# Kernel optimization log

Hardware: AMD Instinct MI355X
Metric: run time of the kernel (lower is better)

The kernel has to match this reference:

```python
import jax, jax.numpy as jnp
import numpy as np

N, E, H, D_IN, D_OUT, DEPTH, G = 100000, 1600000, 128, 128, 10, 3, 256


def setup_inputs() -> dict:
    key = jax.random.key(0)
    ks = jax.random.split(key, 16)
    s = lambda k, shape: jax.random.normal(k, shape, dtype=jnp.float32) * 0.05
    inp = {
        "x": jax.random.normal(ks[0], (N, D_IN), dtype=jnp.float32),
        "edge_index": jax.random.randint(ks[1], (2, E), 0, N, dtype=jnp.int32),
        "control_edge_index": jax.random.randint(ks[2], (2, 1024), 0, N, dtype=jnp.int32),
        "batch": jnp.sort(jax.random.randint(ks[3], (N,), 0, G, dtype=jnp.int32)),
        # encoder MLP: input_dim -> hidden -> hidden
        "enc_w1": s(ks[4], (D_IN, H)), "enc_b1": jnp.zeros((H,), jnp.float32),
        "enc_w2": s(ks[5], (H, H)),    "enc_b2": jnp.zeros((H,), jnp.float32),
        # conv_depth GCN layers, hidden -> hidden
        "conv_w": s(ks[6], (DEPTH, H, H)), "conv_b": jnp.zeros((DEPTH, H), jnp.float32),
        # decoder MLP: hidden -> hidden -> output_dim
        "dec_w1": s(ks[7], (H, H)),     "dec_b1": jnp.zeros((H,), jnp.float32),
        "dec_w2": s(ks[8], (H, D_OUT)), "dec_b2": jnp.zeros((D_OUT,), jnp.float32),
    }
    return inp


def _gcn_forward(x, enc_w1, enc_b1, enc_w2, enc_b2, conv_w, conv_b,
                 dec_w1, dec_b1, dec_w2, dec_b2, edge_index, batch):
    # encoder MLP (Linear-ReLU-Dropout(eval)-Linear)
    h = jax.nn.relu(x @ enc_w1 + enc_b1) @ enc_w2 + enc_b2

    # GCN normalization with self-loops: D^{-1/2} (A + I) D^{-1/2}
    loops = jnp.arange(N, dtype=edge_index.dtype)
    src = jnp.concatenate([edge_index[0], loops])  # [E + N]
    dst = jnp.concatenate([edge_index[1], loops])
    deg = jax.ops.segment_sum(jnp.ones_like(src, dtype=h.dtype), dst, num_segments=N)
    inv_sqrt = jax.lax.rsqrt(deg)  # deg >= 1 thanks to self-loops
    coef = (inv_sqrt[src] * inv_sqrt[dst])[:, None]  # [E+N, 1]

    for l in range(DEPTH):
        hw = h @ conv_w[l] + conv_b[l]                      # [N, H]
        h = jax.ops.segment_sum(hw[src] * coef, dst, num_segments=N)
        if l < DEPTH - 1:  # linear=False -> nonlinearity between convs
            h = jax.nn.relu(h)

    # global_add_pool over graph ids
    pooled = jax.ops.segment_sum(h, batch, num_segments=G)   # [G, H]

    # decoder MLP
    return jax.nn.relu(pooled @ dec_w1 + dec_b1) @ dec_w2 + dec_b2  # [G, D_OUT]


def reference(x, edge_index, control_edge_index, batch, enc_w1, enc_b1, enc_w2,
              enc_b2, conv_w, conv_b, dec_w1, dec_b1, dec_w2, dec_b2):
    # control_edge_index corresponds to the (disabled) control mechanism; unused
    return _gcn_forward(x, enc_w1, enc_b1, enc_w2, enc_b2, conv_w, conv_b,
                        dec_w1, dec_b1, dec_w2, dec_b2, edge_index, batch)
```

## Files before the change

### kernel.cpp

```cpp
#include <hip/hip_runtime.h>
#include <hip/hip_bf16.h>
#include <cstdint>
#include <cstddef>

#define NN 100000
#define NE 1600000
#define HH 128
#define NG 256

#define NB 196
#define BSH 9
#define BMSK 511
#define CHUNK 4096
#define NBLK 391
#define GB 782
#define NBK 391

typedef __bf16 bf16x8 __attribute__((ext_vector_type(8)));
typedef float floatx4 __attribute__((ext_vector_type(4)));

__device__ __forceinline__ uint32_t f2b(float f) {
  union { float f; uint32_t u; } v; v.f = f;
  uint32_t u = v.u;
  return (u + 0x7FFFu + ((u >> 16) & 1u)) >> 16;
}
__device__ __forceinline__ float blo(uint32_t u) {
  union { uint32_t u; float f; } v; v.u = u << 16;
  return v.f;
}
__device__ __forceinline__ float bhi(uint32_t u) {
  union { uint32_t u; float f; } v; v.u = u & 0xFFFF0000u;
  return v.f;
}
__device__ __forceinline__ void addrow(float* a, uint4 v) {
  a[0] += blo(v.x); a[1] += bhi(v.x);
  a[2] += blo(v.y); a[3] += bhi(v.y);
  a[4] += blo(v.z); a[5] += bhi(v.z);
  a[6] += blo(v.w); a[7] += bhi(v.w);
}

__device__ __forceinline__ void stage_w(uint16_t (*Wt)[136], const float* __restrict__ W,
                                        int tid) {
  for (int it = 0; it < 16; ++it) {
    int idx = tid + it * 256;
    int n = idx & 127;
    int k0 = (idx >> 7) * 4;
    uint2 wv;
    wv.x = f2b(W[(k0 + 0) * 128 + n]) | (f2b(W[(k0 + 1) * 128 + n]) << 16);
    wv.y = f2b(W[(k0 + 2) * 128 + n]) | (f2b(W[(k0 + 3) * 128 + n]) << 16);
    *(uint2*)&Wt[n][k0] = wv;
  }
}

__global__ __launch_bounds__(256) void k_front(const int* __restrict__ src,
                                               int* __restrict__ blkcnt,
                                               const float* __restrict__ conv_w,
                                               uint16_t* __restrict__ wbf) {
  int t = threadIdx.x;
  if (blockIdx.x < NBLK) {
    __shared__ int h[NB];
    if (t < NB) h[t] = 0;
    __syncthreads();
    int base = blockIdx.x * CHUNK, end = min(base + CHUNK, NE);
    for (int i = base + t; i < end; i += 256) atomicAdd(&h[src[i] >> BSH], 1);
    __syncthreads();
    if (t < NB) blkcnt[blockIdx.x * NB + t] = h[t];
  } else {
    int idx = (blockIdx.x - NBLK) * 256 + t;
    int l = idx >> 14;
    int n = (idx >> 7) & 127;
    int k = idx & 127;
    wbf[idx] = (uint16_t)f2b(conv_w[(l + 1) * 16384 + k * 128 + n]);
  }
}

__global__ __launch_bounds__(256) void k_cntB(const uint2* __restrict__ pairs,
                                              int* __restrict__ blkcnt) {
  __shared__ int h[NB];
  int t = threadIdx.x;
  if (t < NB) h[t] = 0;
  __syncthreads();
  int base = blockIdx.x * CHUNK, end = min(base + CHUNK, NE);
  for (int i = base + t; i < end; i += 256) atomicAdd(&h[pairs[i].y >> BSH], 1);
  __syncthreads();
  if (t < NB) blkcnt[blockIdx.x * NB + t] = h[t];
}

__global__ void k_scan(const int* __restrict__ blkcnt, int* __restrict__ poff,
                       int* __restrict__ gbase, int* __restrict__ off, int set_off) {
  __shared__ int s[256];
  int t = threadIdx.x;
  int tot = 0;
  if (t < NB) {
    for (int r = 0; r < NBLK; ++r) {
      poff[r * NB + t] = tot;
      tot += blkcnt[r * NB + t];
    }
  }
  s[t] = (t < NB) ? tot : 0;
  __syncthreads();
  for (int d = 1; d < 256; d <<= 1) {
    int v = (t >= d) ? s[t - d] : 0;
    __syncthreads();
    s[t] += v;
    __syncthreads();
  }
  if (t < NB) gbase[t] = s[t] - tot;
  if (t == 0) { gbase[NB] = NE; if (set_off) off[NN] = NE; }
}

__global__ __launch_bounds__(256) void k_placeA(const int* __restrict__ src,
                                                const int* __restrict__ dst,
                                                const int* __restrict__ poff,
                                                const int* __restrict__ gbase,
                                                uint2* __restrict__ pairs) {
  __shared__ int cur[NB];
  int t = threadIdx.x;
  if (t < NB) cur[t] = poff[blockIdx.x * NB + t] + gbase[t];
  __syncthreads();
  int base = blockIdx.x * CHUNK, end = min(base + CHUNK, NE);
  for (int i = base + t; i < end; i += 256) {
    int s = src[i], d = dst[i];
    int p = atomicAdd(&cur[s >> BSH], 1);
    pairs[p] = make_uint2((unsigned)s, (unsigned)d);
  }
}

__global__ __launch_bounds__(256) void k_placeB(const uint2* __restrict__ pairs,
                                                const int* __restrict__ poff,
                                                const int* __restrict__ gbase,
                                                uint32_t* __restrict__ outb) {
  __shared__ int cur[NB];
  int t = threadIdx.x;
  if (t < NB) cur[t] = poff[blockIdx.x * NB + t] + gbase[t];
  __syncthreads();
  int base = blockIdx.x * CHUNK, end = min(base + CHUNK, NE);
  for (int i = base + t; i < end; i += 256) {
    uint2 v = pairs[i];
    int p = atomicAdd(&cur[v.y >> BSH], 1);
    outb[p] = v.x | ((v.y & (unsigned)BMSK) << 17);
  }
}

__global__ __launch_bounds__(256) void k_sortenc(
    const uint32_t* __restrict__ pairbuf, const int* __restrict__ gbase,
    const int* __restrict__ batch,
    int* __restrict__ off, int* __restrict__ csrs,
    int* __restrict__ dhist2, int* __restrict__ gstart,
    const float* __restrict__ A32, const float* __restrict__ W,
    const float* __restrict__ bias, uint16_t* __restrict__ Out)
{
  __shared__ char smraw[34816];
  const int tid = threadIdx.x;

  if (blockIdx.x < GB) {
    auto Wt = (uint16_t(*)[136])smraw;
    stage_w(Wt, W, tid);
    __syncthreads();

    const int lane = tid & 63;
    const int wave = tid >> 6;
    const int lrow = lane & 15;
    const int quad = lane >> 4;
    const int lk = quad * 8;
    const int row0 = blockIdx.x * 128 + wave * 32;

    floatx4 acc[2][8];
#pragma unroll
    for (int t = 0; t < 2; ++t)
#pragma unroll
      for (int n = 0; n < 8; ++n)
        acc[t][n] = (floatx4){0.f, 0.f, 0.f, 0.f};

#pragma unroll
    for (int ks = 0; ks < 4; ++ks) {
      bf16x8 a[2];
#pragma unroll
      for (int t = 0; t < 2; ++t) {
        int r = row0 + t * 16 + lrow;
        uint4 tmp = {0u, 0u, 0u, 0u};
        if (r < NN) {
          float4 f0 = *(const float4*)(A32 + (size_t)r * HH + ks * 32 + lk);
          float4 f1 = *(const float4*)(A32 + (size_t)r * HH + ks * 32 + lk + 4);
          tmp.x = f2b(f0.x) | (f2b(f0.y) << 16);
          tmp.y = f2b(f0.z) | (f2b(f0.w) << 16);
          tmp.z = f2b(f1.x) | (f2b(f1.y) << 16);
          tmp.w = f2b(f1.z) | (f2b(f1.w) << 16);
        }
        a[t] = __builtin_bit_cast(bf16x8, tmp);
      }
#pragma unroll
      for (int n = 0; n < 8; ++n) {
        bf16x8 b = __builtin_bit_cast(bf16x8, *(const uint4*)&Wt[n * 16 + lrow][ks * 32 + lk]);
        acc[0][n] = __builtin_amdgcn_mfma_f32_16x16x32_bf16(b, a[0], acc[0][n], 0, 0, 0);
        acc[1][n] = __builtin_amdgcn_mfma_f32_16x16x32_bf16(b, a[1], acc[1][n], 0, 0, 0);
      }
    }

    float4 b4[8];
#pragma unroll
    for (int n = 0; n < 8; ++n) b4[n] = *(const float4*)(bias + n * 16 + quad * 4);

#pragma unroll
    for (int t = 0; t < 2; ++t) {
      int row = row0 + t * 16 + lrow;
      if (row < NN) {
        uint16_t* orow = Out + (size_t)row * HH;
#pragma unroll
        for (int n = 0; n < 8; ++n) {
          float v0 = fmaxf(acc[t][n][0] + b4[n].x, 0.f);
          float v1 = fmaxf(acc[t][n][1] + b4[n].y, 0.f);
          float v2 = fmaxf(acc[t][n][2] + b4[n].z, 0.f);
          float v3 = fmaxf(acc[t][n][3] + b4[n].w, 0.f);
          uint2 o;
          o.x = f2b(v0) | (f2b(v1) << 16);
          o.y = f2b(v2) | (f2b(v3) << 16);
          *(uint2*)(orow + n * 16 + quad * 4) = o;
        }
      }
    }
  } else {
    int* cnt  = (int*)smraw;
    int* loff = cnt + 512;
    int* psum = loff + 512;
    int b = blockIdx.x - GB;
    cnt[tid] = 0; cnt[tid + 256] = 0;
    __syncthreads();
    int s0 = gbase[b], s1 = gbase[b + 1];
    for (int i = s0 + tid; i < s1; i += 256)
      atomicAdd(&cnt[pairbuf[i] >> 17], 1);
    __syncthreads();
    int a0 = cnt[2 * tid], a1 = cnt[2 * tid + 1];
    int s = a0 + a1;
    psum[tid] = s;
    __syncthreads();
    for (int d = 1; d < 256; d <<= 1) {
      int v = (tid >= d) ? psum[tid - d] : 0;
      __syncthreads();
      psum[tid] += v;
      __syncthreads();
    }
    int excl = psum[tid] - s;
    loff[2 * tid] = excl;
    loff[2 * tid + 1] = excl + a0;
    __syncthreads();
    int* h64 = psum;
    if (tid < 64) h64[tid] = 0;
    __syncthreads();
#pragma unroll
    for (int k = 0; k < 2; ++k) {
      int i = tid + k * 256;
      int node = b * 512 + i;
      if (node < NN) {
        off[node] = s0 + loff[i];
        int d = cnt[i]; if (d > 63) d = 63;
        atomicAdd(&h64[d], 1);
      }
    }
    {
      int n0 = b * 512, n1 = min(n0 + 512, NN);
      for (int i = n0 + tid; i < n1; i += 256) {
        int bb = batch[i];
        if (i == 0) { for (int g = 0; g <= bb; ++g) gstart[g] = 0; }
        else { int aa = batch[i - 1]; for (int g = aa + 1; g <= bb; ++g) gstart[g] = i; }
        if (i == NN - 1) { for (int g = bb + 1; g <= NG; ++g) gstart[g] = NN; }
      }
    }
    __syncthreads();
    if (tid < 64) dhist2[b * 64 + tid] = h64[tid];
    cnt[tid] = loff[tid]; cnt[tid + 256] = loff[tid + 256];
    __syncthreads();
    for (int i = s0 + tid; i < s1; i += 256) {
      uint32_t v = pairbuf[i];
      int p = atomicAdd(&cnt[v >> 17], 1);
      csrs[s0 + p] = (int)(v & 0x1FFFFu);
    }
  }
}

__global__ __launch_bounds__(256) void k_dinv(const int* __restrict__ dhist2,
                                              int* __restrict__ dcur,
                                              const int* __restrict__ off,
                                              float* __restrict__ inv) {
  if (blockIdx.x == 0) {
    int t = threadIdx.x;
    if (t < 64) {
      int sum = 0;
      for (int r = 0; r < NB; ++r) sum += dhist2[r * 64 + (63 - t)];
      int v = sum;
      for (int d = 1; d < 64; d <<= 1) { int u = __shfl_up(v, d); if (t >= d) v += u; }
      dcur[63 - t] = v - sum;
    }
  } else {
    int i = (blockIdx.x - 1) * 256 + threadIdx.x;
    if (i < NN) inv[i] = rsqrtf((float)(off[i + 1] - off[i]) + 1.0f);
  }
}

__global__ __launch_bounds__(256) void k_dualplace(
    const uint16_t* __restrict__ A16,
    const float* __restrict__ Wa, const float* __restrict__ ba,
    const float* __restrict__ Wb, const float* __restrict__ bb,
    const float* __restrict__ scale, uint16_t* __restrict__ Out,
    const int* __restrict__ off, int* __restrict__ dcur, int* __restrict__ order)
{
  __shared__ uint16_t Wt[128][136];
  __shared__ uint16_t tile[128][136];
  const int tid = threadIdx.x;

  if (blockIdx.x < GB) {
    stage_w(Wt, Wa, tid);
    __syncthreads();

    const int lane = tid & 63;
    const int wave = tid >> 6;
    const int lrow = lane & 15;
    const int quad = lane >> 4;
    const int lk = quad * 8;
    const int row0 = blockIdx.x * 128 + wave * 32;
    const int trow0 = wave * 32;

    floatx4 acc[2][8];
#pragma unroll
    for (int t = 0; t < 2; ++t)
#pragma unroll
      for (int n = 0; n < 8; ++n)
        acc[t][n] = (floatx4){0.f, 0.f, 0.f, 0.f};

#pragma unroll
    for (int ks = 0; ks < 4; ++ks) {
      bf16x8 a[2];
#pragma unroll
      for (int t = 0; t < 2; ++t) {
        int r = row0 + t * 16 + lrow;
        uint4 tmp = {0u, 0u, 0u, 0u};
        if (r < NN) tmp = *(const uint4*)(A16 + (size_t)r * HH + ks * 32 + lk);
        a[t] = __builtin_bit_cast(bf16x8, tmp);
      }
#pragma unroll
      for (int n = 0; n < 8; ++n) {
        bf16x8 b = __builtin_bit_cast(bf16x8, *(const uint4*)&Wt[n * 16 + lrow][ks * 32 + lk]);
        acc[0][n] = __builtin_amdgcn_mfma_f32_16x16x32_bf16(b, a[0], acc[0][n], 0, 0, 0);
        acc[1][n] = __builtin_amdgcn_mfma_f32_16x16x32_bf16(b, a[1], acc[1][n], 0, 0, 0);
      }
    }

    {
      float4 b4[8];
#pragma unroll
      for (int n = 0; n < 8; ++n) b4[n] = *(const float4*)(ba + n * 16 + quad * 4);
#pragma unroll
      for (int t = 0; t < 2; ++t) {
        int trow = trow0 + t * 16 + lrow;
#pragma unroll
        for (int n = 0; n < 8; ++n) {
          uint2 o;
          o.x = f2b(acc[t][n][0] + b4[n].x) | (f2b(acc[t][n][1] + b4[n].y) << 16);
          o.y = f2b(acc[t][n][2] + b4[n].z) | (f2b(acc[t][n][3] + b4[n].w) << 16);
          *(uint2*)&tile[trow][n * 16 + quad * 4] = o;
        }
      }
    }
    __syncthreads();
    stage_w(Wt, Wb, tid);
#pragma unroll
    for (int t = 0; t < 2; ++t)
#pragma unroll
      for (int n = 0; n < 8; ++n)
        acc[t][n] = (floatx4){0.f, 0.f, 0.f, 0.f};
    __syncthreads();

#pragma unroll
    for (int ks = 0; ks < 4; ++ks) {
      bf16x8 a[2];
#pragma unroll
      for (int t = 0; t < 2; ++t)
        a[t] = __builtin_bit_cast(bf16x8,
                 *(const uint4*)&tile[trow0 + t * 16 + lrow][ks * 32 + lk]);
#pragma unroll
      for (int n = 0; n < 8; ++n) {
        bf16x8 b = __builtin_bit_cast(bf16x8, *(const uint4*)&Wt[n * 16 + lrow][ks * 32 + lk]);
        acc[0][n] = __builtin_amdgcn_mfma_f32_16x16x32_bf16(b, a[0], acc[0][n], 0, 0, 0);
        acc[1][n] = __builtin_amdgcn_mfma_f32_16x16x32_bf16(b, a[1], acc[1][n], 0, 0, 0);
      }
    }

    {
      float4 b4[8];
#pragma unroll
      for (int n = 0; n < 8; ++n) b4[n] = *(const float4*)(bb + n * 16 + quad * 4);
#pragma unroll
      for (int t = 0; t < 2; ++t) {
        int row = row0 + t * 16 + lrow;
        if (row < NN) {
          float sc = scale[row];
          uint16_t* orow = Out + (size_t)row * HH;
#pragma unroll
          for (int n = 0; n < 8; ++n) {
            float v0 = (acc[t][n][0] + b4[n].x) * sc;
            float v1 = (acc[t][n][1] + b4[n].y) * sc;
            float v2 = (acc[t][n][2] + b4[n].z) * sc;
            float v3 = (acc[t][n][3] + b4[n].w) * sc;
            uint2 o;
            o.x = f2b(v0) | (f2b(v1) << 16);
            o.y = f2b(v2) | (f2b(v3) << 16);
            *(uint2*)(orow + n * 16 + quad * 4) = o;
          }
        }
      }
    }
  } else {
    int* h = (int*)Wt;
    int* base = h + 64;
    if (tid < 64) h[tid] = 0;
    __syncthreads();
    int i = (blockIdx.x - GB) * 256 + tid;
    int d = 0, ld = 0;
    if (i < NN) { d = off[i + 1] - off[i]; if (d > 63) d = 63; ld = atomicAdd(&h[d], 1); }
    __syncthreads();
    if (tid < 64) base[tid] = h[tid] ? atomicAdd(&dcur[tid], h[tid]) : 0;
    __syncthreads();
    if (i < NN) order[base[d] + ld] = i;
  }
}

__global__ __launch_bounds__(256) void k_agg(
    const uint16_t* __restrict__ hw2, const int* __restrict__ off,
    const int* __restrict__ csrs, const float* __restrict__ inv,
    const int* __restrict__ order,
    uint16_t* __restrict__ hout, int do_relu)
{
  int slot = blockIdx.x * 16 + (threadIdx.x >> 4);
  if (slot >= NN) return;
  int node = order[slot];
  int c = (threadIdx.x & 15) * 8;
  const uint16_t* rowp = hw2 + c;

  uint4 sv = *(const uint4*)(rowp + (size_t)node * HH);
  float a[8] = {0.f, 0.f, 0.f, 0.f, 0.f, 0.f, 0.f, 0.f};
  addrow(a, sv);

  int e0 = off[node], e1 = off[node + 1];
  int e = e0;
  for (; e + 4 <= e1; e += 4) {
    int s0 = csrs[e + 0], s1 = csrs[e + 1], s2 = csrs[e + 2], s3 = csrs[e + 3];
    uint4 v0 = *(const uint4*)(rowp + (size_t)s0 * HH);
    uint4 v1 = *(const uint4*)(rowp + (size_t)s1 * HH);
    uint4 v2 = *(const uint4*)(rowp + (size_t)s2 * HH);
    uint4 v3 = *(const uint4*)(rowp + (size_t)s3 * HH);
    addrow(a, v0); addrow(a, v1); addrow(a, v2); addrow(a, v3);
  }
  for (; e < e1; ++e) {
    int s = csrs[e];
    uint4 v = *(const uint4*)(rowp + (size_t)s * HH);
    addrow(a, v);
  }
  float invd = inv[node];
#pragma unroll
  for (int j = 0; j < 8; ++j) {
    a[j] *= invd;
    if (do_relu) a[j] = fmaxf(a[j], 0.f);
  }
  uint4 o;
  o.x = f2b(a[0]) | (f2b(a[1]) << 16);
  o.y = f2b(a[2]) | (f2b(a[3]) << 16);
  o.z = f2b(a[4]) | (f2b(a[5]) << 16);
  o.w = f2b(a[6]) | (f2b(a[7]) << 16);
  *(uint4*)(hout + (size_t)node * HH + c) = o;
}

__global__ __launch_bounds__(512) void k_aggemm(
    const uint16_t* __restrict__ hw2, const int* __restrict__ off,
    const int* __restrict__ csrs, const float* __restrict__ inv,
    const int* __restrict__ order,
    const uint16_t* __restrict__ Wbf, const float* __restrict__ bias,
    uint16_t* __restrict__ Out)
{
  __shared__ uint4 S4[32][16];
  __shared__ int nid[32];
  const int tid = threadIdx.x;

  const int group = tid >> 4;
  const int node = order[blockIdx.x * 32 + group];
  const int c = (tid & 15) * 8;
  if ((tid & 15) == 0) nid[group] = node;
  const uint16_t* rowp = hw2 + c;

  uint4 sv = *(const uint4*)(rowp + (size_t)node * HH);
  float a[8] = {0.f, 0.f, 0.f, 0.f, 0.f, 0.f, 0.f, 0.f};
  addrow(a, sv);

  int e0 = off[node], e1 = off[node + 1];
  int e = e0;
  for (; e + 4 <= e1; e += 4) {
    int s0 = csrs[e + 0], s1 = csrs[e + 1], s2 = csrs[e + 2], s3 = csrs[e + 3];
    uint4 v0 = *(const uint4*)(rowp + (size_t)s0 * HH);
    uint4 v1 = *(const uint4*)(rowp + (size_t)s1 * HH);
    uint4 v2 = *(const uint4*)(rowp + (size_t)s2 * HH);
    uint4 v3 = *(const uint4*)(rowp + (size_t)s3 * HH);
    addrow(a, v0); addrow(a, v1); addrow(a, v2); addrow(a, v3);
  }
  for (; e < e1; ++e) {
    int s = csrs[e];
    uint4 v = *(const uint4*)(rowp + (size_t)s * HH);
    addrow(a, v);
  }
  float invd = inv[node];
#pragma unroll
  for (int j = 0; j < 8; ++j) a[j] = fmaxf(a[j] * invd, 0.f);
  {
    uint4 o;
    o.x = f2b(a[0]) | (f2b(a[1]) << 16);
    o.y = f2b(a[2]) | (f2b(a[3]) << 16);
    o.z = f2b(a[4]) | (f2b(a[5]) << 16);
    o.w = f2b(a[6]) | (f2b(a[7]) << 16);
    S4[group][(tid & 15) ^ (group & 15)] = o;
  }
  __syncthreads();

  const int lane = tid & 63;
  const int wave = tid >> 6;
  const int lrow = lane & 15;
  const int quad = lane >> 4;
  const int lk = quad * 8;
  const uint16_t* wrow = Wbf + (size_t)(wave * 16 + lrow) * HH;

  floatx4 acc0 = (floatx4){0.f, 0.f, 0.f, 0.f};
  floatx4 acc1 = (floatx4){0.f, 0.f, 0.f, 0.f};
#pragma unroll
  for (int ks = 0; ks < 4; ++ks) {
    int ch = (ks * 4 + quad) ^ lrow;
    bf16x8 a0 = __builtin_bit_cast(bf16x8, S4[lrow][ch]);
    bf16x8 a1 = __builtin_bit_cast(bf16x8, S4[16 + lrow][ch]);
    bf16x8 b  = __builtin_bit_cast(bf16x8, *(const uint4*)(wrow + ks * 32 + lk));
    acc0 = __builtin_amdgcn_mfma_f32_16x16x32_bf16(b, a0, acc0, 0, 0, 0);
    acc1 = __builtin_amdgcn_mfma_f32_16x16x32_bf16(b, a1, acc1, 0, 0, 0);
  }

  float4 b4 = *(const float4*)(bias + wave * 16 + quad * 4);
#pragma unroll
  for (int t = 0; t < 2; ++t) {
    floatx4 ac = t ? acc1 : acc0;
    int row = nid[t * 16 + lrow];
    float sc = inv[row];
    float v0 = (ac[0] + b4.x) * sc;
    float v1 = (ac[1] + b4.y) * sc;
    float v2 = (ac[2] + b4.z) * sc;
    float v3 = (ac[3] + b4.w) * sc;
    uint2 o;
    o.x = f2b(v0) | (f2b(v1) << 16);
    o.y = f2b(v2) | (f2b(v3) << 16);
    *(uint2*)(Out + (size_t)row * HH + wave * 16 + quad * 4) = o;
  }
}

__global__ __launch_bounds__(256) void k_pooldec(
    const uint16_t* __restrict__ h, const int* __restrict__ gstart,
    const float* __restrict__ w1, const float* __restrict__ b1,
    const float* __restrict__ w2, const float* __restrict__ b2,
    float* __restrict__ out)
{
  __shared__ float red[16][132];
  __shared__ float p[128], tmpv[128];
  int g = blockIdx.x;
  int tid = threadIdx.x;
  int slot = tid >> 4;
  int c = (tid & 15) * 8;

  int r0 = gstart[g], r1 = gstart[g + 1];
  float a[8] = {0.f, 0.f, 0.f, 0.f, 0.f, 0.f, 0.f, 0.f};
  for (int r = r0 + slot; r < r1; r += 16) {
    uint4 v = *(const uint4*)(h + (size_t)r * HH + c);
    addrow(a, v);
  }
  *(float4*)&red[slot][c]     = make_float4(a[0], a[1], a[2], a[3]);
  *(float4*)&red[slot][c + 4] = make_float4(a[4], a[5], a[6], a[7]);
  __syncthreads();
  if (tid < 128) {
    float s = 0.f;
#pragma unroll
    for (int k = 0; k < 16; ++k) s += red[k][tid];
    p[tid] = s;
  }
  __syncthreads();
  if (tid < 128) {
    float acc1 = b1[tid];
    for (int k = 0; k < 128; ++k) acc1 += p[k] * w1[k * 128 + tid];
    tmpv[tid] = fmaxf(acc1, 0.f);
  }
  __syncthreads();
  if (tid < 10) {
    float o = b2[tid];
    for (int k = 0; k < 128; ++k) o += tmpv[k] * w2[k * 10 + tid];
    out[g * 10 + tid] = o;
  }
}

extern "C" void kernel_launch(void* const* d_in, const int* in_sizes, int n_in,
                              void* d_out, int out_size, void* d_ws, size_t ws_size,
                              hipStream_t stream) {
  const float* x       = (const float*)d_in[0];
  const int*   eidx    = (const int*)d_in[1];
  const int*   src     = eidx;
  const int*   dst     = eidx + NE;
  const int*   batch   = (const int*)d_in[3];
  const float* enc_w1  = (const float*)d_in[4];
  const float* enc_b1  = (const float*)d_in[5];
  const float* enc_w2  = (const float*)d_in[6];
  const float* enc_b2  = (const float*)d_in[7];
  const float* conv_w  = (const float*)d_in[8];
  const float* conv_b  = (const float*)d_in[9];
  const float* dec_w1  = (const float*)d_in[10];
  const float* dec_b1  = (const float*)d_in[11];
  const float* dec_w2  = (const float*)d_in[12];
  const float* dec_b2  = (const float*)d_in[13];
  float* out = (float*)d_out;

  char* ws = (char*)d_ws;
  size_t o = 0;
  auto alloc = [&](size_t bytes) -> char* {
    char* p = ws + o;
    o += (bytes + 255) & ~(size_t)255;
    return p;
  };
  int*      off     = (int*)alloc((size_t)(NN + 1) * 4);
  int*      csrs    = (int*)alloc((size_t)NE * 4);
  float*    inv     = (float*)alloc((size_t)NN * 4);
  int*      blkcntA = (int*)alloc((size_t)NBLK * NB * 4);
  int*      poffA   = (int*)alloc((size_t)NBLK * NB * 4);
  int*      blkcntB = (int*)alloc((size_t)NBLK * NB * 4);
  int*      poffB   = (int*)alloc((size_t)NBLK * NB * 4);
  int*      gbaseA  = (int*)alloc((size_t)(NB + 1) * 4);
  int*      gbaseB  = (int*)alloc((size_t)(NB + 1) * 4);
  int*      dhist2  = (int*)alloc((size_t)NB * 64 * 4);
  int*      dcur    = (int*)alloc(64 * 4);
  int*      order   = (int*)alloc((size_t)NN * 4);
  int*      gstart  = (int*)alloc((size_t)(NG + 1) * 4);
  uint16_t* wbf     = (uint16_t*)alloc((size_t)2 * 16384 * 2);
  uint32_t* pairB   = (uint32_t*)alloc((size_t)NE * 4);
  uint16_t* buf0    = (uint16_t*)alloc((size_t)NN * HH * 2);
  uint16_t* buf1    = (uint16_t*)alloc((size_t)NN * HH * 2);
  uint2*    pairsA  = (uint2*)buf1;

  k_front<<<dim3(NBLK + 128), dim3(256), 0, stream>>>(src, blkcntA, conv_w, wbf);
  k_scan<<<dim3(1), dim3(256), 0, stream>>>(blkcntA, poffA, gbaseA, off, 0);
  k_placeA<<<dim3(NBLK), dim3(256), 0, stream>>>(src, dst, poffA, gbaseA, pairsA);
  k_cntB<<<dim3(NBLK), dim3(256), 0, stream>>>(pairsA, blkcntB);
  k_scan<<<dim3(1), dim3(256), 0, stream>>>(blkcntB, poffB, gbaseB, off, 1);
  k_placeB<<<dim3(NBLK), dim3(256), 0, stream>>>(pairsA, poffB, gbaseB, pairB);
  k_sortenc<<<dim3(GB + NB), dim3(256), 0, stream>>>(pairB, gbaseB, batch, off, csrs,
                                                     dhist2, gstart,
                                                     x, enc_w1, enc_b1, buf1);
  k_dinv<<<dim3(1 + NBK), dim3(256), 0, stream>>>(dhist2, dcur, off, inv);
  k_dualplace<<<dim3(GB + NBK), dim3(256), 0, stream>>>(buf1, enc_w2, enc_b2,
                                                        conv_w + 0 * 16384, conv_b + 0,
                                                        inv, buf0, off, dcur, order);

  const int FB = NN / 32;
  const int AB = (NN + 15) / 16;
  k_aggemm<<<dim3(FB), dim3(512), 0, stream>>>(buf0, off, csrs, inv, order,
                                               wbf, conv_b + 128, buf1);
  k_aggemm<<<dim3(FB), dim3(512), 0, stream>>>(buf1, off, csrs, inv, order,
                                               wbf + 16384, conv_b + 256, buf0);
  k_agg <<<dim3(AB), dim3(256), 0, stream>>>(buf0, off, csrs, inv, order, buf1, 0);

  k_pooldec<<<dim3(NG), dim3(256), 0, stream>>>(buf1, gstart, dec_w1, dec_b1, dec_w2, dec_b2, out);
}
```

Baseline: 484.5 us.

## Fuse final aggregation with global add pooling via atomics; preload MFMA weights

The last GCN aggregation now accumulates directly into a float pooled buffer. Each block of 16 consecutive nodes forms per-graph partial sums in shared memory and adds them with atomics, so the bf16 write and re-read of the final node features is gone. The pooled buffer is zeroed inside the front kernel, and the decoder kernel now only reads the pooled rows. Separately, k_aggemm loads its weight fragments into registers before the gather phase so their latency overlaps the gather. The trade-offs are float atomics with nondeterministic summation order, and the loss of degree-sorted node ordering in the last aggregation.

```diff
diff --git a/kernel.cpp b/kernel.cpp
--- a/kernel.cpp
+++ b/kernel.cpp
@@ -55,7 +55,8 @@
 __global__ __launch_bounds__(256) void k_front(const int* __restrict__ src,
                                                int* __restrict__ blkcnt,
                                                const float* __restrict__ conv_w,
-                                               uint16_t* __restrict__ wbf) {
+                                               uint16_t* __restrict__ wbf,
+                                               float* __restrict__ pooled) {
   int t = threadIdx.x;
   if (blockIdx.x < NBLK) {
     __shared__ int h[NB];
@@ -65,12 +66,15 @@
     for (int i = base + t; i < end; i += 256) atomicAdd(&h[src[i] >> BSH], 1);
     __syncthreads();
     if (t < NB) blkcnt[blockIdx.x * NB + t] = h[t];
-  } else {
+  } else if (blockIdx.x < NBLK + 128) {
     int idx = (blockIdx.x - NBLK) * 256 + t;
     int l = idx >> 14;
     int n = (idx >> 7) & 127;
     int k = idx & 127;
     wbf[idx] = (uint16_t)f2b(conv_w[(l + 1) * 16384 + k * 128 + n]);
+  } else {
+    int i = ((blockIdx.x - NBLK - 128) * 256 + t) * 4;
+    if (i < NG * HH) *(float4*)&pooled[i] = make_float4(0.f, 0.f, 0.f, 0.f);
   }
 }
 
@@ -424,51 +428,6 @@
   }
 }
 
-__global__ __launch_bounds__(256) void k_agg(
-    const uint16_t* __restrict__ hw2, const int* __restrict__ off,
-    const int* __restrict__ csrs, const float* __restrict__ inv,
-    const int* __restrict__ order,
-    uint16_t* __restrict__ hout, int do_relu)
-{
-  int slot = blockIdx.x * 16 + (threadIdx.x >> 4);
-  if (slot >= NN) return;
-  int node = order[slot];
-  int c = (threadIdx.x & 15) * 8;
-  const uint16_t* rowp = hw2 + c;
-
-  uint4 sv = *(const uint4*)(rowp + (size_t)node * HH);
-  float a[8] = {0.f, 0.f, 0.f, 0.f, 0.f, 0.f, 0.f, 0.f};
-  addrow(a, sv);
-
-  int e0 = off[node], e1 = off[node + 1];
-  int e = e0;
-  for (; e + 4 <= e1; e += 4) {
-    int s0 = csrs[e + 0], s1 = csrs[e + 1], s2 = csrs[e + 2], s3 = csrs[e + 3];
-    uint4 v0 = *(const uint4*)(rowp + (size_t)s0 * HH);
-    uint4 v1 = *(const uint4*)(rowp + (size_t)s1 * HH);
-    uint4 v2 = *(const uint4*)(rowp + (size_t)s2 * HH);
-    uint4 v3 = *(const uint4*)(rowp + (size_t)s3 * HH);
-    addrow(a, v0); addrow(a, v1); addrow(a, v2); addrow(a, v3);
-  }
-  for (; e < e1; ++e) {
-    int s = csrs[e];
-    uint4 v = *(const uint4*)(rowp + (size_t)s * HH);
-    addrow(a, v);
-  }
-  float invd = inv[node];
-#pragma unroll
-  for (int j = 0; j < 8; ++j) {
-    a[j] *= invd;
-    if (do_relu) a[j] = fmaxf(a[j], 0.f);
-  }
-  uint4 o;
-  o.x = f2b(a[0]) | (f2b(a[1]) << 16);
-  o.y = f2b(a[2]) | (f2b(a[3]) << 16);
-  o.z = f2b(a[4]) | (f2b(a[5]) << 16);
-  o.w = f2b(a[6]) | (f2b(a[7]) << 16);
-  *(uint4*)(hout + (size_t)node * HH + c) = o;
-}
-
 __global__ __launch_bounds__(512) void k_aggemm(
     const uint16_t* __restrict__ hw2, const int* __restrict__ off,
     const int* __restrict__ csrs, const float* __restrict__ inv,
@@ -479,6 +438,17 @@
   __shared__ uint4 S4[32][16];
   __shared__ int nid[32];
   const int tid = threadIdx.x;
+  const int lane = tid & 63;
+  const int wave = tid >> 6;
+  const int lrow = lane & 15;
+  const int quad = lane >> 4;
+  const int lk = quad * 8;
+
+  const uint16_t* wrow = Wbf + (size_t)(wave * 16 + lrow) * HH;
+  uint4 w0 = *(const uint4*)(wrow + 0 * 32 + lk);
+  uint4 w1 = *(const uint4*)(wrow + 1 * 32 + lk);
+  uint4 w2 = *(const uint4*)(wrow + 2 * 32 + lk);
+  uint4 w3 = *(const uint4*)(wrow + 3 * 32 + lk);
 
   const int group = tid >> 4;
   const int node = order[blockIdx.x * 32 + group];
@@ -518,13 +488,6 @@
   }
   __syncthreads();
 
-  const int lane = tid & 63;
-  const int wave = tid >> 6;
-  const int lrow = lane & 15;
-  const int quad = lane >> 4;
-  const int lk = quad * 8;
-  const uint16_t* wrow = Wbf + (size_t)(wave * 16 + lrow) * HH;
-
   floatx4 acc0 = (floatx4){0.f, 0.f, 0.f, 0.f};
   floatx4 acc1 = (floatx4){0.f, 0.f, 0.f, 0.f};
 #pragma unroll
@@ -532,7 +495,8 @@
     int ch = (ks * 4 + quad) ^ lrow;
     bf16x8 a0 = __builtin_bit_cast(bf16x8, S4[lrow][ch]);
     bf16x8 a1 = __builtin_bit_cast(bf16x8, S4[16 + lrow][ch]);
-    bf16x8 b  = __builtin_bit_cast(bf16x8, *(const uint4*)(wrow + ks * 32 + lk));
+    uint4 wv = (ks == 0) ? w0 : (ks == 1) ? w1 : (ks == 2) ? w2 : w3;
+    bf16x8 b  = __builtin_bit_cast(bf16x8, wv);
     acc0 = __builtin_amdgcn_mfma_f32_16x16x32_bf16(b, a0, acc0, 0, 0, 0);
     acc1 = __builtin_amdgcn_mfma_f32_16x16x32_bf16(b, a1, acc1, 0, 0, 0);
   }
@@ -554,34 +518,72 @@
   }
 }
 
-__global__ __launch_bounds__(256) void k_pooldec(
-    const uint16_t* __restrict__ h, const int* __restrict__ gstart,
+__global__ __launch_bounds__(256) void k_aggpool(
+    const uint16_t* __restrict__ hw2, const int* __restrict__ off,
+    const int* __restrict__ csrs, const float* __restrict__ inv,
+    const int* __restrict__ batch,
+    float* __restrict__ pooled)
+{
+  __shared__ float red[16][132];
+  __shared__ int gid[16];
+  const int tid = threadIdx.x;
+  const int slot = tid >> 4;
+  const int node = blockIdx.x * 16 + slot;
+  const int c = (tid & 15) * 8;
+  if ((tid & 15) == 0) gid[slot] = batch[node];
+  const uint16_t* rowp = hw2 + c;
+
+  uint4 sv = *(const uint4*)(rowp + (size_t)node * HH);
+  float a[8] = {0.f, 0.f, 0.f, 0.f, 0.f, 0.f, 0.f, 0.f};
+  addrow(a, sv);
+
+  int e0 = off[node], e1 = off[node + 1];
+  int e = e0;
+  for (; e + 4 <= e1; e += 4) {
+    int s0 = csrs[e + 0], s1 = csrs[e + 1], s2 = csrs[e + 2], s3 = csrs[e + 3];
+    uint4 v0 = *(const uint4*)(rowp + (size_t)s0 * HH);
+    uint4 v1 = *(const uint4*)(rowp + (size_t)s1 * HH);
+    uint4 v2 = *(const uint4*)(rowp + (size_t)s2 * HH);
+    uint4 v3 = *(const uint4*)(rowp + (size_t)s3 * HH);
+    addrow(a, v0); addrow(a, v1); addrow(a, v2); addrow(a, v3);
+  }
+  for (; e < e1; ++e) {
+    int s = csrs[e];
+    uint4 v = *(const uint4*)(rowp + (size_t)s * HH);
+    addrow(a, v);
+  }
+  float invd = inv[node];
+#pragma unroll
+  for (int j = 0; j < 8; ++j) a[j] *= invd;
+  *(float4*)&red[slot][c]     = make_float4(a[0], a[1], a[2], a[3]);
+  *(float4*)&red[slot][c + 4] = make_float4(a[4], a[5], a[6], a[7]);
+  __syncthreads();
+
+  if (tid < 128) {
+    int g = gid[0];
+    float run = red[0][tid];
+    for (int r = 1; r < 16; ++r) {
+      int gg = gid[r];
+      if (gg != g) {
+        unsafeAtomicAdd(&pooled[(size_t)g * HH + tid], run);
+        run = 0.f; g = gg;
+      }
+      run += red[r][tid];
+    }
+    unsafeAtomicAdd(&pooled[(size_t)g * HH + tid], run);
+  }
+}
+
+__global__ __launch_bounds__(256) void k_dec(
+    const float* __restrict__ pooled,
     const float* __restrict__ w1, const float* __restrict__ b1,
     const float* __restrict__ w2, const float* __restrict__ b2,
     float* __restrict__ out)
 {
-  __shared__ float red[16][132];
   __shared__ float p[128], tmpv[128];
   int g = blockIdx.x;
   int tid = threadIdx.x;
-  int slot = tid >> 4;
-  int c = (tid & 15) * 8;
-
-  int r0 = gstart[g], r1 = gstart[g + 1];
-  float a[8] = {0.f, 0.f, 0.f, 0.f, 0.f, 0.f, 0.f, 0.f};
-  for (int r = r0 + slot; r < r1; r += 16) {
-    uint4 v = *(const uint4*)(h + (size_t)r * HH + c);
-    addrow(a, v);
-  }
-  *(float4*)&red[slot][c]     = make_float4(a[0], a[1], a[2], a[3]);
-  *(float4*)&red[slot][c + 4] = make_float4(a[4], a[5], a[6], a[7]);
-  __syncthreads();
-  if (tid < 128) {
-    float s = 0.f;
-#pragma unroll
-    for (int k = 0; k < 16; ++k) s += red[k][tid];
-    p[tid] = s;
-  }
+  if (tid < 128) p[tid] = pooled[(size_t)g * HH + tid];
   __syncthreads();
   if (tid < 128) {
     float acc1 = b1[tid];
@@ -636,13 +638,14 @@
   int*      dcur    = (int*)alloc(64 * 4);
   int*      order   = (int*)alloc((size_t)NN * 4);
   int*      gstart  = (int*)alloc((size_t)(NG + 1) * 4);
+  float*    pooled  = (float*)alloc((size_t)NG * HH * 4);
   uint16_t* wbf     = (uint16_t*)alloc((size_t)2 * 16384 * 2);
   uint32_t* pairB   = (uint32_t*)alloc((size_t)NE * 4);
   uint16_t* buf0    = (uint16_t*)alloc((size_t)NN * HH * 2);
   uint16_t* buf1    = (uint16_t*)alloc((size_t)NN * HH * 2);
   uint2*    pairsA  = (uint2*)buf1;
 
-  k_front<<<dim3(NBLK + 128), dim3(256), 0, stream>>>(src, blkcntA, conv_w, wbf);
+  k_front<<<dim3(NBLK + 128 + 32), dim3(256), 0, stream>>>(src, blkcntA, conv_w, wbf, pooled);
   k_scan<<<dim3(1), dim3(256), 0, stream>>>(blkcntA, poffA, gbaseA, off, 0);
   k_placeA<<<dim3(NBLK), dim3(256), 0, stream>>>(src, dst, poffA, gbaseA, pairsA);
   k_cntB<<<dim3(NBLK), dim3(256), 0, stream>>>(pairsA, blkcntB);
@@ -657,12 +660,12 @@
                                                         inv, buf0, off, dcur, order);
 
   const int FB = NN / 32;
-  const int AB = (NN + 15) / 16;
+  const int AB = NN / 16;
   k_aggemm<<<dim3(FB), dim3(512), 0, stream>>>(buf0, off, csrs, inv, order,
                                                wbf, conv_b + 128, buf1);
   k_aggemm<<<dim3(FB), dim3(512), 0, stream>>>(buf1, off, csrs, inv, order,
                                                wbf + 16384, conv_b + 256, buf0);
-  k_agg <<<dim3(AB), dim3(256), 0, stream>>>(buf0, off, csrs, inv, order, buf1, 0);
-
-  k_pooldec<<<dim3(NG), dim3(256), 0, stream>>>(buf1, gstart, dec_w1, dec_b1, dec_w2, dec_b2, out);
-}
+  k_aggpool<<<dim3(AB), dim3(256), 0, stream>>>(buf0, off, csrs, inv, batch, pooled);
+
+  k_dec<<<dim3(NG), dim3(256), 0, stream>>>(pooled, dec_w1, dec_b1, dec_w2, dec_b2, out);
+}
```

Measured after the change: 485.2 us. No clear change (+0.2%).
